# Optimization experiments

Hardware: AMD Instinct MI355X
Metric: run time of the kernel (lower is better)

## Reference

```python
import jax, jax.numpy as jnp
import numpy as np

EMBED_DIM = 1024
B, S = 4, 4096


def setup_inputs() -> dict:
    key = jax.random.key(0)
    kx, kq, kk, kv = jax.random.split(key, 4)
    x = jax.random.normal(kx, (B, S, EMBED_DIM), dtype=jnp.float32)
    W_Q = jax.random.normal(kq, (EMBED_DIM, EMBED_DIM), dtype=jnp.float32)
    W_K = jax.random.normal(kk, (EMBED_DIM, EMBED_DIM), dtype=jnp.float32)
    W_V = jax.random.normal(kv, (EMBED_DIM, EMBED_DIM), dtype=jnp.float32)
    return {"x": x, "W_Q": W_Q, "W_K": W_K, "W_V": W_V}


def reference(x, W_Q, W_K, W_V):
    # Q, K, V: [B, S, D]
    Q = x @ W_Q
    K = x @ W_K
    V = x @ W_V
    scale = 1.0 / jnp.sqrt(jnp.float32(EMBED_DIM))
    # scores: [B, S, S] (full score matrix, as in the original)
    scores = jnp.einsum('bsd,btd->bst', Q, K) * scale
    attn = jax.nn.softmax(scores, axis=-1)
    # output: [B, S, D]
    Z = jnp.einsum('bst,btd->bsd', attn, V)
    return Z
```

## Files before the change

kernel.cpp:

```cpp
#include <hip/hip_runtime.h>


typedef _Float16 half8 __attribute__((ext_vector_type(8)));
typedef _Float16 half4v __attribute__((ext_vector_type(4)));
typedef float floatx4 __attribute__((ext_vector_type(4)));

__device__ __forceinline__ void glds16(const _Float16* g, _Float16* l) {
    __builtin_amdgcn_global_load_lds(
        (const __attribute__((address_space(1))) void*)g,
        (__attribute__((address_space(3))) void*)l, 16, 0, 0);
}

template <bool SPLITIN, int OMODE, bool PMAX>
__global__ __launch_bounds__(256, 2) void gemm_nt(
    const _Float16* __restrict__ AH, const _Float16* __restrict__ AL,
    const _Float16* BH, const _Float16* BL,
    void* out0, void* out1,
    const float* __restrict__ rdiv, float* __restrict__ pmax,
    float scale, int M, int N, int K,
    const _Float16* BH2, const _Float16* BL2, void* o0b, void* o1b)
{
    if (blockIdx.z == 1) { BH = BH2; BL = BL2; out0 = o0b; out1 = o1b; }

    __shared__ _Float16 sAH[128 * 32];
    __shared__ _Float16 sBH[128 * 32];
    __shared__ _Float16 sAL[SPLITIN ? 128 * 32 : 8];
    __shared__ _Float16 sBL[SPLITIN ? 128 * 32 : 8];

    const int tid = threadIdx.x;
    const int bm = blockIdx.y, bn = blockIdx.x;
    const int lane = tid & 63, quad = lane >> 4, lrow = lane & 15;
    const int wave = tid >> 6, wm = wave >> 1, wn = wave & 1;

    const int wb = (tid & 192) * 8;
    const size_t g0 = (size_t)(tid >> 2) * K + (tid & 3) * 8;
    const size_t g1 = (size_t)((256 + tid) >> 2) * K + (tid & 3) * 8;
    const _Float16* pA0 = AH + (size_t)bm * 128 * K + g0;
    const _Float16* pA1 = AH + (size_t)bm * 128 * K + g1;
    const _Float16* pB0 = BH + (size_t)bn * 128 * K + g0;
    const _Float16* pB1 = BH + (size_t)bn * 128 * K + g1;
    const _Float16* pA0L = SPLITIN ? (AL + (size_t)bm * 128 * K + g0) : nullptr;
    const _Float16* pA1L = SPLITIN ? (AL + (size_t)bm * 128 * K + g1) : nullptr;
    const _Float16* pB0L = SPLITIN ? (BL + (size_t)bn * 128 * K + g0) : nullptr;
    const _Float16* pB1L = SPLITIN ? (BL + (size_t)bn * 128 * K + g1) : nullptr;

    floatx4 acc[4][4] = {};

    const int aoff = (wm * 64 + lrow) * 32 + quad * 8;
    const int boff = (wn * 64 + lrow) * 32 + quad * 8;

    for (int k0 = 0; k0 < K; k0 += 32) {
        glds16(pA0, sAH + wb);        glds16(pA1, sAH + 2048 + wb);
        glds16(pB0, sBH + wb);        glds16(pB1, sBH + 2048 + wb);
        if (SPLITIN) {
            glds16(pA0L, sAL + wb);   glds16(pA1L, sAL + 2048 + wb);
            glds16(pB0L, sBL + wb);   glds16(pB1L, sBL + 2048 + wb);
        }
        pA0 += 32; pA1 += 32; pB0 += 32; pB1 += 32;
        if (SPLITIN) { pA0L += 32; pA1L += 32; pB0L += 32; pB1L += 32; }
        __syncthreads();

        half8 aH[4], bH[4], aL[4], bL[4];
        #pragma unroll
        for (int i = 0; i < 4; ++i) {
            aH[i] = *(const half8*)&sAH[aoff + i * 16 * 32];
            bH[i] = *(const half8*)&sBH[boff + i * 16 * 32];
            if (SPLITIN) {
                aL[i] = *(const half8*)&sAL[aoff + i * 16 * 32];
                bL[i] = *(const half8*)&sBL[boff + i * 16 * 32];
            }
        }
        #pragma unroll
        for (int mi = 0; mi < 4; ++mi)
            #pragma unroll
            for (int nj = 0; nj < 4; ++nj) {
                acc[mi][nj] = __builtin_amdgcn_mfma_f32_16x16x32_f16(
                    aH[mi], bH[nj], acc[mi][nj], 0, 0, 0);
                if (SPLITIN) {
                    acc[mi][nj] = __builtin_amdgcn_mfma_f32_16x16x32_f16(
                        aH[mi], bL[nj], acc[mi][nj], 0, 0, 0);
                    acc[mi][nj] = __builtin_amdgcn_mfma_f32_16x16x32_f16(
                        aL[mi], bH[nj], acc[mi][nj], 0, 0, 0);
                }
            }
        __syncthreads();
    }

    #pragma unroll
    for (int mi = 0; mi < 4; ++mi) {
        #pragma unroll
        for (int r = 0; r < 4; ++r) {
            const int grow = bm * 128 + wm * 64 + mi * 16 + quad * 4 + r;
            float s = scale;
            if (OMODE == 1) s = scale / rdiv[grow];
            float v[4];
            #pragma unroll
            for (int nj = 0; nj < 4; ++nj) v[nj] = acc[mi][nj][r] * s;
            if (PMAX) {
                float mx = fmaxf(fmaxf(v[0], v[1]), fmaxf(v[2], v[3]));
                #pragma unroll
                for (int off = 1; off < 16; off <<= 1)
                    mx = fmaxf(mx, __shfl_xor(mx, off));
                if (lrow == 0) pmax[(size_t)grow * 64 + bn * 2 + wn] = mx;
            }
            #pragma unroll
            for (int nj = 0; nj < 4; ++nj) {
                const int gcol = bn * 128 + wn * 64 + nj * 16 + lrow;
                const size_t idx = (size_t)grow * N + gcol;
                if (OMODE <= 1) {
                    ((float*)out0)[idx] = v[nj];
                } else if (OMODE == 2) {
                    ((_Float16*)out0)[idx] = (_Float16)v[nj];
                } else {
                    const _Float16 h = (_Float16)v[nj];
                    ((_Float16*)out0)[idx] = h;
                    ((_Float16*)out1)[idx] = (_Float16)(v[nj] - (float)h);
                }
            }
        }
    }
}

__global__ __launch_bounds__(256) void split_scale(
    const float* __restrict__ x, _Float16* __restrict__ hi,
    _Float16* __restrict__ lo, int n)
{
    int i = (blockIdx.x * 256 + threadIdx.x) * 4;
    const int stride = gridDim.x * 256 * 4;
    for (; i < n; i += stride) {
        float4 v = *(const float4*)(x + i);
        float a[4] = {v.x * 256.f, v.y * 256.f, v.z * 256.f, v.w * 256.f};
        half4v h, l;
        #pragma unroll
        for (int j = 0; j < 4; ++j) {
            h[j] = (_Float16)a[j];
            l[j] = (_Float16)(a[j] - (float)h[j]);
        }
        *(half4v*)(hi + i) = h;
        *(half4v*)(lo + i) = l;
    }
}

__global__ __launch_bounds__(256) void wprep3(
    const float* __restrict__ W0, const float* __restrict__ W1,
    const float* __restrict__ W2,
    _Float16* __restrict__ h0, _Float16* __restrict__ l0,
    _Float16* __restrict__ h1, _Float16* __restrict__ l1,
    _Float16* __restrict__ h2, int dim)
{
    const int z = blockIdx.z;
    const float* W = (z == 0) ? W0 : (z == 1) ? W1 : W2;
    _Float16* hiT = (z == 0) ? h0 : (z == 1) ? h1 : h2;
    _Float16* loT = (z == 0) ? l0 : (z == 1) ? l1 : nullptr;

    __shared__ float t[32][33];
    const int n0 = blockIdx.x * 32, k0 = blockIdx.y * 32;
    const int tx = threadIdx.x, ty = threadIdx.y;
    #pragma unroll
    for (int i = 0; i < 4; ++i)
        t[ty + 8 * i][tx] = 256.f * W[(size_t)(k0 + ty + 8 * i) * dim + n0 + tx];
    __syncthreads();
    #pragma unroll
    for (int i = 0; i < 4; ++i) {
        const int nn = ty + 8 * i;
        const float v = t[tx][nn];
        const _Float16 h = (_Float16)v;
        const size_t o = (size_t)(n0 + nn) * dim + k0 + tx;
        hiT[o] = h;
        if (loT) loT[o] = (_Float16)(v - (float)h);
    }
}

__global__ __launch_bounds__(256) void softmax_p(
    const float* __restrict__ Sc, const float* __restrict__ pmax,
    _Float16* __restrict__ P, float* __restrict__ rowsum)
{
    __shared__ float red[8];
    const int tid = threadIdx.x;
    const int row = blockIdx.x;
    const float* srow = Sc + (size_t)row * 4096;
    _Float16* prow = P + (size_t)row * 4096;

    if (tid < 64) {
        float m = pmax[(size_t)row * 64 + tid];
        #pragma unroll
        for (int off = 32; off; off >>= 1) m = fmaxf(m, __shfl_xor(m, off));
        if (tid == 0) red[0] = m;
    }
    __syncthreads();
    const float rmax = red[0];

    float s = 0.f;
    for (int c = tid * 4; c < 4096; c += 1024) {
        float4 v = *(const float4*)(srow + c);
        float p0 = __expf(v.x - rmax), p1 = __expf(v.y - rmax);
        float p2 = __expf(v.z - rmax), p3 = __expf(v.w - rmax);
        s += p0 + p1 + p2 + p3;
        half4v h = {(_Float16)p0, (_Float16)p1, (_Float16)p2, (_Float16)p3};
        *(half4v*)(prow + c) = h;
    }
    #pragma unroll
    for (int off = 32; off; off >>= 1) s += __shfl_xor(s, off, 64);
    if ((tid & 63) == 0) red[4 + (tid >> 6)] = s;
    __syncthreads();
    if (tid == 0) rowsum[row] = red[4] + red[5] + red[6] + red[7];
}

extern "C" void kernel_launch(void* const* d_in, const int* in_sizes, int n_in,
                              void* d_out, int out_size, void* d_ws, size_t ws_size,
                              hipStream_t stream) {
    const int Bb = 4, S = 4096, D = 1024;
    const size_t SD = (size_t)S * D;
    const size_t SS = (size_t)S * S;

    const float* x  = (const float*)d_in[0];
    const float* WQ = (const float*)d_in[1];
    const float* WK = (const float*)d_in[2];
    const float* WV = (const float*)d_in[3];
    float* out = (float*)d_out;

    char* w = (char*)d_ws;
    _Float16* WQhT = (_Float16*)w;  w += (size_t)D * D * 2;
    _Float16* WQlT = (_Float16*)w;  w += (size_t)D * D * 2;
    _Float16* WKhT = (_Float16*)w;  w += (size_t)D * D * 2;
    _Float16* WKlT = (_Float16*)w;  w += (size_t)D * D * 2;
    _Float16* WvhT = (_Float16*)w;  w += (size_t)D * D * 2;
    _Float16* xhi  = (_Float16*)w;  w += SD * 2;
    _Float16* xlo  = (_Float16*)w;  w += SD * 2;
    _Float16* Qhi  = (_Float16*)w;  w += SD * 2;
    _Float16* Qlo  = (_Float16*)w;  w += SD * 2;
    _Float16* Khi  = (_Float16*)w;  w += SD * 2;
    _Float16* Klo  = (_Float16*)w;  w += SD * 2;
    _Float16* VT   = (_Float16*)w;  w += SD * 2;
    float*    rowsum = (float*)w;   w += (size_t)S * 4;
    float*    pmax = (float*)w;     w += (size_t)S * 64 * 4;
    float*    Sc   = (float*)w;     w += SS * 4;
    _Float16* P    = (_Float16*)w;  w += SS * 2;

    const float kInv256 = 0.00390625f;
    const float kScScale = 4.76837158203125e-7f;

    dim3 blk(256);

    wprep3<<<dim3(32, 32, 3), dim3(32, 8), 0, stream>>>(
        WQ, WK, WV, WQhT, WQlT, WKhT, WKlT, WvhT, D);

    for (int b = 0; b < Bb; ++b) {
        const float* xb = x + (size_t)b * SD;
        float* outb = out + (size_t)b * SD;

        split_scale<<<dim3(4096), blk, 0, stream>>>(xb, xhi, xlo, (int)SD);

        gemm_nt<true, 3, false><<<dim3(D / 128, S / 128, 2), blk, 0, stream>>>(
            xhi, xlo, WQhT, WQlT, Qhi, Qlo, nullptr, nullptr, kInv256, S, D, D,
            WKhT, WKlT, Khi, Klo);

        gemm_nt<false, 2, false><<<dim3(S / 128, D / 128, 1), blk, 0, stream>>>(
            WvhT, nullptr, xhi, nullptr, VT, nullptr, nullptr, nullptr, kInv256,
            D, S, D, nullptr, nullptr, nullptr, nullptr);

        gemm_nt<true, 0, true><<<dim3(S / 128, S / 128, 1), blk, 0, stream>>>(
            Qhi, Qlo, Khi, Klo, Sc, nullptr, nullptr, pmax, kScScale, S, S, D,
            nullptr, nullptr, nullptr, nullptr);

        softmax_p<<<dim3(S), blk, 0, stream>>>(Sc, pmax, P, rowsum);

        gemm_nt<false, 1, false><<<dim3(D / 128, S / 128, 1), blk, 0, stream>>>(
            P, nullptr, VT, nullptr, outb, nullptr, rowsum, nullptr, kInv256,
            S, D, S, nullptr, nullptr, nullptr, nullptr);
    }
}
```

Before: 1.312 ms.

## Double-buffer LDS tiles in GEMM to overlap global loads with MFMA

The shared-memory tiles for A and B (and their low-precision split parts) are doubled so the next K-tile is prefetched with global_load_lds while MFMAs run on the current tile. This also drops the trailing barrier, leaving one __syncthreads per K-step. The goal is to hide global-load latency behind compute. The cost is twice the LDS per block, which can limit occupancy. Correctness depends on the barrier waiting for the outstanding LDS-DMA loads.

Measured after the change: 1.275 ms. 2.8% less time.

```diff
diff --git a/kernel.cpp b/kernel.cpp
--- a/kernel.cpp
+++ b/kernel.cpp
@@ -22,10 +22,10 @@
 {
     if (blockIdx.z == 1) { BH = BH2; BL = BL2; out0 = o0b; out1 = o1b; }
 
-    __shared__ _Float16 sAH[128 * 32];
-    __shared__ _Float16 sBH[128 * 32];
-    __shared__ _Float16 sAL[SPLITIN ? 128 * 32 : 8];
-    __shared__ _Float16 sBL[SPLITIN ? 128 * 32 : 8];
+    __shared__ _Float16 sAH[2 * 128 * 32];
+    __shared__ _Float16 sBH[2 * 128 * 32];
+    __shared__ _Float16 sAL[SPLITIN ? 2 * 128 * 32 : 8];
+    __shared__ _Float16 sBL[SPLITIN ? 2 * 128 * 32 : 8];
 
     const int tid = threadIdx.x;
     const int bm = blockIdx.y, bn = blockIdx.x;
@@ -49,25 +49,40 @@
     const int aoff = (wm * 64 + lrow) * 32 + quad * 8;
     const int boff = (wn * 64 + lrow) * 32 + quad * 8;
 
+    glds16(pA0, sAH + wb);        glds16(pA1, sAH + 2048 + wb);
+    glds16(pB0, sBH + wb);        glds16(pB1, sBH + 2048 + wb);
+    if (SPLITIN) {
+        glds16(pA0L, sAL + wb);   glds16(pA1L, sAL + 2048 + wb);
+        glds16(pB0L, sBL + wb);   glds16(pB1L, sBL + 2048 + wb);
+    }
+    pA0 += 32; pA1 += 32; pB0 += 32; pB1 += 32;
+    if (SPLITIN) { pA0L += 32; pA1L += 32; pB0L += 32; pB1L += 32; }
+
+    int cur = 0;
     for (int k0 = 0; k0 < K; k0 += 32) {
-        glds16(pA0, sAH + wb);        glds16(pA1, sAH + 2048 + wb);
-        glds16(pB0, sBH + wb);        glds16(pB1, sBH + 2048 + wb);
-        if (SPLITIN) {
-            glds16(pA0L, sAL + wb);   glds16(pA1L, sAL + 2048 + wb);
-            glds16(pB0L, sBL + wb);   glds16(pB1L, sBL + 2048 + wb);
-        }
-        pA0 += 32; pA1 += 32; pB0 += 32; pB1 += 32;
-        if (SPLITIN) { pA0L += 32; pA1L += 32; pB0L += 32; pB1L += 32; }
         __syncthreads();
 
+        if (k0 + 32 < K) {
+            const int nb = (cur ^ 1) * 4096;
+            glds16(pA0, sAH + nb + wb);        glds16(pA1, sAH + nb + 2048 + wb);
+            glds16(pB0, sBH + nb + wb);        glds16(pB1, sBH + nb + 2048 + wb);
+            if (SPLITIN) {
+                glds16(pA0L, sAL + nb + wb);   glds16(pA1L, sAL + nb + 2048 + wb);
+                glds16(pB0L, sBL + nb + wb);   glds16(pB1L, sBL + nb + 2048 + wb);
+            }
+            pA0 += 32; pA1 += 32; pB0 += 32; pB1 += 32;
+            if (SPLITIN) { pA0L += 32; pA1L += 32; pB0L += 32; pB1L += 32; }
+        }
+
+        const int cb = cur * 4096;
         half8 aH[4], bH[4], aL[4], bL[4];
         #pragma unroll
         for (int i = 0; i < 4; ++i) {
-            aH[i] = *(const half8*)&sAH[aoff + i * 16 * 32];
-            bH[i] = *(const half8*)&sBH[boff + i * 16 * 32];
+            aH[i] = *(const half8*)&sAH[cb + aoff + i * 16 * 32];
+            bH[i] = *(const half8*)&sBH[cb + boff + i * 16 * 32];
             if (SPLITIN) {
-                aL[i] = *(const half8*)&sAL[aoff + i * 16 * 32];
-                bL[i] = *(const half8*)&sBL[boff + i * 16 * 32];
+                aL[i] = *(const half8*)&sAL[cb + aoff + i * 16 * 32];
+                bL[i] = *(const half8*)&sBL[cb + boff + i * 16 * 32];
             }
         }
         #pragma unroll
@@ -83,7 +98,7 @@
                         aL[mi], bH[nj], acc[mi][nj], 0, 0, 0);
                 }
             }
-        __syncthreads();
+        cur ^= 1;
     }
 
     #pragma unroll
```
